# Optimization experiments

Measured on AMD Instinct MI355X. Metric: run time of the kernel, lower is better.

The kernel has to match this reference:

```python
import jax, jax.numpy as jnp
import numpy as np

N_NODES = 50000
N_EDGES = 800000
IN_DIM = 128
HIDDEN = 128
NUM_CLASSES = 2
NUM_GRAPHS = 512


def _linear_params(key, fan_in, fan_out):
    # torch nn.Linear default init: U(-1/sqrt(fan_in), 1/sqrt(fan_in))
    k1, k2 = jax.random.split(key)
    bound = 1.0 / np.sqrt(fan_in)
    W = jax.random.uniform(k1, (fan_in, fan_out), jnp.float32, -bound, bound)
    b = jax.random.uniform(k2, (fan_out,), jnp.float32, -bound, bound)
    return W, b


def setup_inputs() -> dict:
    key = jax.random.key(0)
    ks = jax.random.split(key, 8)
    x = jax.random.normal(ks[0], (N_NODES, IN_DIM), jnp.float32)
    edge_index = jax.random.randint(ks[1], (2, N_EDGES), 0, N_NODES, jnp.int64)
    batch = jnp.sort(jax.random.randint(ks[2], (N_NODES,), 0, NUM_GRAPHS, jnp.int64))
    W1a, b1a = _linear_params(ks[3], IN_DIM, HIDDEN)
    W1b, b1b = _linear_params(ks[4], HIDDEN, HIDDEN)
    W2a, b2a = _linear_params(ks[5], HIDDEN, HIDDEN)
    W2b, b2b = _linear_params(ks[6], HIDDEN, HIDDEN)
    Wfc, bfc = _linear_params(ks[7], HIDDEN, NUM_CLASSES)
    return {"x": x, "edge_index": edge_index, "batch": batch,
            "W1a": W1a, "b1a": b1a, "W1b": W1b, "b1b": b1b,
            "W2a": W2a, "b2a": b2a, "W2b": W2b, "b2b": b2b,
            "Wfc": Wfc, "bfc": bfc}


def _gin_layer(x, src, dst, Wa, ba, Wb, bb):
    # GINConv (eps=0): h_i = MLP(x_i + sum_{j->i} x_j)
    agg = jax.ops.segment_sum(x[src], dst, num_segments=N_NODES)
    h = x + agg
    h = jax.nn.relu(h @ Wa + ba)
    h = h @ Wb + bb
    return jax.nn.relu(h)  # outer F.relu in forward; dropout is identity (eval)


def reference(x, edge_index, batch, W1a, b1a, W1b, b1b, W2a, b2a, W2b, b2b, Wfc, bfc):
    src, dst = edge_index[0], edge_index[1]
    h = _gin_layer(x, src, dst, W1a, b1a, W1b, b1b)
    h = _gin_layer(h, src, dst, W2a, b2a, W2b, b2b)
    # global mean pool per graph
    sums = jax.ops.segment_sum(h, batch, num_segments=NUM_GRAPHS)
    counts = jax.ops.segment_sum(jnp.ones((N_NODES,), h.dtype), batch, num_segments=NUM_GRAPHS)
    g_emb = sums / jnp.maximum(counts, 1.0)[:, None]
    return g_emb @ Wfc + bfc  # [NUM_GRAPHS, NUM_CLASSES]
```

## Files before the change

### kernel.cpp

```cpp
#include <hip/hip_runtime.h>

typedef unsigned short ushort_t;
typedef unsigned int uint_t;

typedef __bf16 bf16x8 __attribute__((ext_vector_type(8)));
typedef float f32x4 __attribute__((ext_vector_type(4)));

#define N_NODES 50000
#define N_EDGES 800000
#define DIM 128
#define NUM_GRAPHS 512
#define LDA 136

#define ELL_CAP 64

#define NBUCK 256
#define BUCK_SZ 196
#define FIFO_CAP 4096
#define A_CHUNK 2048
#define A_BLOCKS ((N_EDGES + A_CHUNK - 1) / A_CHUNK)

#define PREP_X_BLOCKS 6250
#define PREP_W_BLOCKS 256
#define PREP_B_BLOCKS 196
#define PREP_TOTAL (A_BLOCKS + PREP_X_BLOCKS + PREP_W_BLOCKS + PREP_B_BLOCKS + 1)

__device__ __forceinline__ float bf2f(ushort_t u) {
    return __uint_as_float(((uint_t)u) << 16);
}
__device__ __forceinline__ ushort_t f2bf(float f) {
    uint_t u = __float_as_uint(f);
    u = (u + 0x7FFF + ((u >> 16) & 1)) >> 16;
    return (ushort_t)u;
}
__device__ __forceinline__ bf16x8 as_bf16x8(uint4 v) {
    return __builtin_bit_cast(bf16x8, v);
}

__global__ void zero_detect_kernel(float* gsum, int* gcnt, const void* xraw,
                                   const void* eiraw, int* flags) {
    int i = blockIdx.x * 256 + threadIdx.x;
    if (i < NUM_GRAPHS * DIM) gsum[i] = 0.f;
    if (i < NBUCK) gcnt[i] = 0;
    if (i == 0) {
        const ushort_t* u = (const ushort_t*)xraw;
        int extreme = 0;
        for (int k = 0; k < 128; ++k) {
            int e = (u[k] >> 7) & 0xFF;
            if (e >= 0xC0) extreme++;
        }
        flags[0] = (extreme > 8) ? 1 : 0;
        const int* p = (const int*)eiraw;
        int nonzero = 0;
        for (int k = 1; k < 64; k += 2) nonzero += (p[k] != 0);
        flags[1] = (nonzero == 0) ? 1 : 0;
    }
}

__global__ __launch_bounds__(256) void prep_all_kernel(
    const void* xraw, const void* braw, const void* eiraw,
    const void* W0, const void* W1, const void* W2, const void* W3,
    const void* pb1a, const void* pb1b, const void* pb2a, const void* pb2b,
    const void* pWfc, const void* pbfc, const int* __restrict__ flags,
    ushort_t* __restrict__ xout, ushort_t* __restrict__ wpout,
    int* __restrict__ batch32, float* __restrict__ params,
    int* __restrict__ gcnt, uint_t* __restrict__ fifo) {
    __shared__ int lcnt[NBUCK];
    __shared__ int lbase[NBUCK];
    int b = blockIdx.x;
    int tid = threadIdx.x;
    if (b < A_BLOCKS) {
        lcnt[tid] = 0;
        __syncthreads();
        const int* p = (const int*)eiraw;
        int i64 = flags[1];
        int base_e = b * A_CHUNK;
        int gk[8], rk[8];
        uint_t pk[8];
#pragma unroll
        for (int k = 0; k < 8; ++k) {
            int e = base_e + k * 256 + tid;
            int valid = e < N_EDGES;
            int s = 0, d = 0;
            if (valid) {
                if (i64) { s = p[2 * e]; d = p[2 * (N_EDGES + e)]; }
                else     { s = p[e];     d = p[N_EDGES + e]; }
            }
            int g = d / BUCK_SZ;
            gk[k] = valid ? g : -1;
            pk[k] = (uint_t)s | ((uint_t)(d - g * BUCK_SZ) << 16);
            rk[k] = valid ? atomicAdd(&lcnt[g], 1) : 0;
        }
        __syncthreads();
        lbase[tid] = atomicAdd(&gcnt[tid], lcnt[tid]);
        __syncthreads();
#pragma unroll
        for (int k = 0; k < 8; ++k) {
            if (gk[k] >= 0) {
                int pos = lbase[gk[k]] + rk[k];
                if (pos < FIFO_CAP)
                    fifo[(size_t)gk[k] * FIFO_CAP + pos] = pk[k];
            }
        }
    } else if (b < A_BLOCKS + PREP_X_BLOCKS) {
        if (flags[0]) {
            int i = (b - A_BLOCKS) * 256 + tid;
            if (i < N_NODES * DIM / 4) {
                float4 v = ((const float4*)xraw)[i];
                ushort4 o;
                o.x = f2bf(v.x); o.y = f2bf(v.y); o.z = f2bf(v.z); o.w = f2bf(v.w);
                ((ushort4*)xout)[i] = o;
            }
        }
    } else if (b < A_BLOCKS + PREP_X_BLOCKS + PREP_W_BLOCKS) {
        int gidx = (b - A_BLOCKS - PREP_X_BLOCKS) * 256 + tid;
        int which = gidx >> 14;
        const void* W = (which == 0) ? W0 : (which == 1) ? W1 : (which == 2) ? W2 : W3;
        int idx = gidx & 16383;
        int j = idx & 7;
        int L = (idx >> 3) & 63;
        int t = (idx >> 9) & 7;
        int s = idx >> 12;
        int k = s * 32 + (L >> 4) * 8 + j;
        int n = t * 16 + (L & 15);
        int off = k * DIM + n;
        wpout[gidx] = flags[0] ? f2bf(((const float*)W)[off]) : ((const ushort_t*)W)[off];
    } else if (b < A_BLOCKS + PREP_X_BLOCKS + PREP_W_BLOCKS + PREP_B_BLOCKS) {
        int i = (b - A_BLOCKS - PREP_X_BLOCKS - PREP_W_BLOCKS) * 256 + tid;
        if (i < N_NODES) {
            const int* p = (const int*)braw;
            batch32[i] = flags[1] ? p[2 * i] : p[i];
        }
    } else {
        for (int i = tid; i < 770; i += 256) {
            const void* srcp;
            int j;
            if (i < 128)      { srcp = pb1a; j = i; }
            else if (i < 256) { srcp = pb1b; j = i - 128; }
            else if (i < 384) { srcp = pb2a; j = i - 256; }
            else if (i < 512) { srcp = pb2b; j = i - 384; }
            else if (i < 768) { srcp = pWfc; j = i - 512; }
            else              { srcp = pbfc; j = i - 768; }
            params[i] = flags[0] ? ((const float*)srcp)[j] : bf2f(((const ushort_t*)srcp)[j]);
        }
    }
}

__global__ __launch_bounds__(256) void scatter_kernel(const uint_t* __restrict__ fifo,
                                                      const int* __restrict__ gcnt,
                                                      int* __restrict__ cnt,
                                                      int* __restrict__ ell) {
    __shared__ int lcnt[BUCK_SZ];
    int b = blockIdx.x;
    int tid = threadIdx.x;
    if (tid < BUCK_SZ) lcnt[tid] = 0;
    __syncthreads();
    int n = gcnt[b];
    if (n > FIFO_CAP) n = FIFO_CAP;
    const uint_t* f = fifo + (size_t)b * FIFO_CAP;
    int node0 = b * BUCK_SZ;
    for (int i = tid; i < n; i += 256) {
        uint_t e = f[i];
        int s = (int)(e & 0xFFFFu);
        int dl = (int)(e >> 16);
        int slot = atomicAdd(&lcnt[dl], 1);
        if (slot < ELL_CAP) ell[(size_t)(node0 + dl) * ELL_CAP + slot] = s;
    }
    __syncthreads();
    if (tid < BUCK_SZ) {
        int node = node0 + tid;
        if (node < N_NODES) cnt[node] = lcnt[tid];
    }
}

__global__ __launch_bounds__(256) void agg_kernel(const ushort_t* __restrict__ featA,
                                                  const void* __restrict__ featB,
                                                  const int* __restrict__ flags,
                                                  const int* __restrict__ deg,
                                                  const int* __restrict__ ell,
                                                  ushort_t* __restrict__ hout) {
    int n = blockIdx.x * 16 + (threadIdx.x >> 4);
    int lane = threadIdx.x & 15;
    if (n >= N_NODES) return;
    const ushort_t* feat = featA;
    if (flags && !flags[0]) feat = (const ushort_t*)featB;
    const uint4* fp = reinterpret_cast<const uint4*>(feat);
    uint4 v = fp[(size_t)n * 16 + lane];
    float a0 = bf2f((ushort_t)(v.x & 0xffff));
    float a1 = bf2f((ushort_t)(v.x >> 16));
    float a2 = bf2f((ushort_t)(v.y & 0xffff));
    float a3 = bf2f((ushort_t)(v.y >> 16));
    float a4 = bf2f((ushort_t)(v.z & 0xffff));
    float a5 = bf2f((ushort_t)(v.z >> 16));
    float a6 = bf2f((ushort_t)(v.w & 0xffff));
    float a7 = bf2f((ushort_t)(v.w >> 16));
    int e1 = deg[n];
    if (e1 > ELL_CAP) e1 = ELL_CAP;
    const int4* __restrict__ rp4 = reinterpret_cast<const int4*>(ell + (size_t)n * ELL_CAP);
    const int* __restrict__ row = ell + (size_t)n * ELL_CAP;
    int j = 0;
#define ACC8(V) \
    a0 += bf2f((ushort_t)((V).x & 0xffff)); a1 += bf2f((ushort_t)((V).x >> 16)); \
    a2 += bf2f((ushort_t)((V).y & 0xffff)); a3 += bf2f((ushort_t)((V).y >> 16)); \
    a4 += bf2f((ushort_t)((V).z & 0xffff)); a5 += bf2f((ushort_t)((V).z >> 16)); \
    a6 += bf2f((ushort_t)((V).w & 0xffff)); a7 += bf2f((ushort_t)((V).w >> 16));
    for (; j + 8 <= e1; j += 8) {
        int4 ra = rp4[j >> 2];
        int4 rb = rp4[(j >> 2) + 1];
        uint4 g0 = fp[(size_t)ra.x * 16 + lane];
        uint4 g1 = fp[(size_t)ra.y * 16 + lane];
        uint4 g2 = fp[(size_t)ra.z * 16 + lane];
        uint4 g3 = fp[(size_t)ra.w * 16 + lane];
        uint4 g4 = fp[(size_t)rb.x * 16 + lane];
        uint4 g5 = fp[(size_t)rb.y * 16 + lane];
        uint4 g6 = fp[(size_t)rb.z * 16 + lane];
        uint4 g7 = fp[(size_t)rb.w * 16 + lane];
        ACC8(g0) ACC8(g1) ACC8(g2) ACC8(g3)
        ACC8(g4) ACC8(g5) ACC8(g6) ACC8(g7)
    }
    for (; j + 4 <= e1; j += 4) {
        int4 ra = rp4[j >> 2];
        uint4 g0 = fp[(size_t)ra.x * 16 + lane];
        uint4 g1 = fp[(size_t)ra.y * 16 + lane];
        uint4 g2 = fp[(size_t)ra.z * 16 + lane];
        uint4 g3 = fp[(size_t)ra.w * 16 + lane];
        ACC8(g0) ACC8(g1) ACC8(g2) ACC8(g3)
    }
    for (; j < e1; ++j) {
        int s = row[j];
        uint4 g0 = fp[(size_t)s * 16 + lane];
        ACC8(g0)
    }
#undef ACC8
    uint4 o;
    o.x = (uint_t)f2bf(a0) | ((uint_t)f2bf(a1) << 16);
    o.y = (uint_t)f2bf(a2) | ((uint_t)f2bf(a3) << 16);
    o.z = (uint_t)f2bf(a4) | ((uint_t)f2bf(a5) << 16);
    o.w = (uint_t)f2bf(a6) | ((uint_t)f2bf(a7) << 16);
    reinterpret_cast<uint4*>(hout)[(size_t)n * 16 + lane] = o;
}

__global__ __launch_bounds__(256) void mlp_kernel(const ushort_t* __restrict__ hin,
                                                  const ushort_t* __restrict__ wpA,
                                                  const float* __restrict__ ba,
                                                  const ushort_t* __restrict__ wpB,
                                                  const float* __restrict__ bb,
                                                  ushort_t* __restrict__ hout) {
    __shared__ ushort_t As[64 * LDA];
    int tid = threadIdx.x;
    int wave = tid >> 6;
    int lane = tid & 63;
    int quad = lane >> 4;
    int cl = lane & 15;
    int row0 = blockIdx.x * 64;

    bf16x8 B1[2][4], B2[2][4];
#pragma unroll
    for (int ti = 0; ti < 2; ++ti) {
        int t = 2 * wave + ti;
#pragma unroll
        for (int s = 0; s < 4; ++s) {
            B1[ti][s] = as_bf16x8(reinterpret_cast<const uint4*>(wpA)[(s * 8 + t) * 64 + lane]);
            B2[ti][s] = as_bf16x8(reinterpret_cast<const uint4*>(wpB)[(s * 8 + t) * 64 + lane]);
        }
    }

    for (int i = tid; i < 64 * 16; i += 256) {
        int r = i >> 4, c8 = i & 15;
        uint4 v = make_uint4(0u, 0u, 0u, 0u);
        int gr = row0 + r;
        if (gr < N_NODES)
            v = reinterpret_cast<const uint4*>(hin + (size_t)gr * DIM)[c8];
        *reinterpret_cast<uint4*>(&As[r * LDA + c8 * 8]) = v;
    }
    __syncthreads();

    f32x4 acc[4][2];
#pragma unroll
    for (int m = 0; m < 4; ++m)
#pragma unroll
        for (int ti = 0; ti < 2; ++ti)
#pragma unroll
            for (int r = 0; r < 4; ++r) acc[m][ti][r] = 0.f;

#pragma unroll
    for (int s = 0; s < 4; ++s) {
#pragma unroll
        for (int m = 0; m < 4; ++m) {
            bf16x8 a = *reinterpret_cast<const bf16x8*>(&As[(m * 16 + cl) * LDA + s * 32 + quad * 8]);
#pragma unroll
            for (int ti = 0; ti < 2; ++ti)
                acc[m][ti] = __builtin_amdgcn_mfma_f32_16x16x32_bf16(a, B1[ti][s], acc[m][ti], 0, 0, 0);
        }
    }
    __syncthreads();

#pragma unroll
    for (int ti = 0; ti < 2; ++ti) {
        int col = 32 * wave + ti * 16 + cl;
        float bv = ba[col];
#pragma unroll
        for (int m = 0; m < 4; ++m)
#pragma unroll
            for (int r = 0; r < 4; ++r) {
                float v = acc[m][ti][r] + bv;
                As[(m * 16 + quad * 4 + r) * LDA + col] = f2bf(fmaxf(v, 0.f));
            }
    }
    __syncthreads();

#pragma unroll
    for (int m = 0; m < 4; ++m)
#pragma unroll
        for (int ti = 0; ti < 2; ++ti)
#pragma unroll
            for (int r = 0; r < 4; ++r) acc[m][ti][r] = 0.f;

#pragma unroll
    for (int s = 0; s < 4; ++s) {
#pragma unroll
        for (int m = 0; m < 4; ++m) {
            bf16x8 a = *reinterpret_cast<const bf16x8*>(&As[(m * 16 + cl) * LDA + s * 32 + quad * 8]);
#pragma unroll
            for (int ti = 0; ti < 2; ++ti)
                acc[m][ti] = __builtin_amdgcn_mfma_f32_16x16x32_bf16(a, B2[ti][s], acc[m][ti], 0, 0, 0);
        }
    }

#pragma unroll
    for (int ti = 0; ti < 2; ++ti) {
        int col = 32 * wave + ti * 16 + cl;
        float bv = bb[col];
#pragma unroll
        for (int m = 0; m < 4; ++m)
#pragma unroll
            for (int r = 0; r < 4; ++r) {
                int gr = row0 + m * 16 + quad * 4 + r;
                if (gr < N_NODES) {
                    float v = acc[m][ti][r] + bv;
                    hout[(size_t)gr * DIM + col] = f2bf(fmaxf(v, 0.f));
                }
            }
    }
}

__global__ __launch_bounds__(256) void mlp_pool_kernel(const ushort_t* __restrict__ hin,
                                                       const ushort_t* __restrict__ wpA,
                                                       const float* __restrict__ ba,
                                                       const ushort_t* __restrict__ wpB,
                                                       const float* __restrict__ bb,
                                                       const int* __restrict__ batch32,
                                                       float* __restrict__ gsum) {
    __shared__ ushort_t As[64 * LDA];
    int tid = threadIdx.x;
    int wave = tid >> 6;
    int lane = tid & 63;
    int quad = lane >> 4;
    int cl = lane & 15;
    int row0 = blockIdx.x * 64;

    bf16x8 B1[2][4], B2[2][4];
#pragma unroll
    for (int ti = 0; ti < 2; ++ti) {
        int t = 2 * wave + ti;
#pragma unroll
        for (int s = 0; s < 4; ++s) {
            B1[ti][s] = as_bf16x8(reinterpret_cast<const uint4*>(wpA)[(s * 8 + t) * 64 + lane]);
            B2[ti][s] = as_bf16x8(reinterpret_cast<const uint4*>(wpB)[(s * 8 + t) * 64 + lane]);
        }
    }

    for (int i = tid; i < 64 * 16; i += 256) {
        int r = i >> 4, c8 = i & 15;
        uint4 v = make_uint4(0u, 0u, 0u, 0u);
        int gr = row0 + r;
        if (gr < N_NODES)
            v = reinterpret_cast<const uint4*>(hin + (size_t)gr * DIM)[c8];
        *reinterpret_cast<uint4*>(&As[r * LDA + c8 * 8]) = v;
    }
    __syncthreads();

    f32x4 acc[4][2];
#pragma unroll
    for (int m = 0; m < 4; ++m)
#pragma unroll
        for (int ti = 0; ti < 2; ++ti)
#pragma unroll
            for (int r = 0; r < 4; ++r) acc[m][ti][r] = 0.f;

#pragma unroll
    for (int s = 0; s < 4; ++s) {
#pragma unroll
        for (int m = 0; m < 4; ++m) {
            bf16x8 a = *reinterpret_cast<const bf16x8*>(&As[(m * 16 + cl) * LDA + s * 32 + quad * 8]);
#pragma unroll
            for (int ti = 0; ti < 2; ++ti)
                acc[m][ti] = __builtin_amdgcn_mfma_f32_16x16x32_bf16(a, B1[ti][s], acc[m][ti], 0, 0, 0);
        }
    }
    __syncthreads();

#pragma unroll
    for (int ti = 0; ti < 2; ++ti) {
        int col = 32 * wave + ti * 16 + cl;
        float bv = ba[col];
#pragma unroll
        for (int m = 0; m < 4; ++m)
#pragma unroll
            for (int r = 0; r < 4; ++r) {
                float v = acc[m][ti][r] + bv;
                As[(m * 16 + quad * 4 + r) * LDA + col] = f2bf(fmaxf(v, 0.f));
            }
    }
    __syncthreads();

#pragma unroll
    for (int m = 0; m < 4; ++m)
#pragma unroll
        for (int ti = 0; ti < 2; ++ti)
#pragma unroll
            for (int r = 0; r < 4; ++r) acc[m][ti][r] = 0.f;

#pragma unroll
    for (int s = 0; s < 4; ++s) {
#pragma unroll
        for (int m = 0; m < 4; ++m) {
            bf16x8 a = *reinterpret_cast<const bf16x8*>(&As[(m * 16 + cl) * LDA + s * 32 + quad * 8]);
#pragma unroll
            for (int ti = 0; ti < 2; ++ti)
                acc[m][ti] = __builtin_amdgcn_mfma_f32_16x16x32_bf16(a, B2[ti][s], acc[m][ti], 0, 0, 0);
        }
    }
    __syncthreads();

#pragma unroll
    for (int ti = 0; ti < 2; ++ti) {
        int col = 32 * wave + ti * 16 + cl;
        float bv = bb[col];
#pragma unroll
        for (int m = 0; m < 4; ++m)
#pragma unroll
            for (int r = 0; r < 4; ++r) {
                float v = acc[m][ti][r] + bv;
                As[(m * 16 + quad * 4 + r) * LDA + col] = f2bf(fmaxf(v, 0.f));
            }
    }
    __syncthreads();

    int c = tid & 127;
    int rbase = (tid >> 7) * 32;
    float accp = 0.f;
    int curg = -1;
    for (int r = rbase; r < rbase + 32; ++r) {
        int gr = row0 + r;
        if (gr >= N_NODES) break;
        int g = batch32[gr];
        if (g != curg) {
            if (curg >= 0) atomicAdd(&gsum[curg * DIM + c], accp);
            curg = g;
            accp = 0.f;
        }
        accp += bf2f(As[r * LDA + c]);
    }
    if (curg >= 0) atomicAdd(&gsum[curg * DIM + c], accp);
}

__global__ __launch_bounds__(64) void fc_kernel(const float* __restrict__ gsum,
                                                const int* __restrict__ batch,
                                                const float* __restrict__ params,
                                                const int* __restrict__ flags,
                                                void* __restrict__ out) {
    int g = blockIdx.x;
    int l = threadIdx.x;
    int lo = 0, hi = N_NODES;
    while (lo < hi) { int mid = (lo + hi) >> 1; if (batch[mid] < g) lo = mid + 1; else hi = mid; }
    int start = lo;
    hi = N_NODES;
    while (lo < hi) { int mid = (lo + hi) >> 1; if (batch[mid] < g + 1) lo = mid + 1; else hi = mid; }
    int cnt = lo - start;
    float inv = 1.0f / (float)(cnt > 0 ? cnt : 1);
    float m0 = gsum[g * DIM + l] * inv;
    float m1 = gsum[g * DIM + 64 + l] * inv;
    float p0 = m0 * params[512 + l * 2 + 0] + m1 * params[512 + (64 + l) * 2 + 0];
    float p1 = m0 * params[512 + l * 2 + 1] + m1 * params[512 + (64 + l) * 2 + 1];
#pragma unroll
    for (int off = 32; off > 0; off >>= 1) {
        p0 += __shfl_down(p0, off, 64);
        p1 += __shfl_down(p1, off, 64);
    }
    if (l == 0) {
        float o0 = p0 + params[768];
        float o1 = p1 + params[769];
        if (flags[0]) {
            ((float*)out)[g * 2 + 0] = o0;
            ((float*)out)[g * 2 + 1] = o1;
        } else {
            ((ushort_t*)out)[g * 2 + 0] = f2bf(o0);
            ((ushort_t*)out)[g * 2 + 1] = f2bf(o1);
        }
    }
}

extern "C" void kernel_launch(void* const* d_in, const int* in_sizes, int n_in,
                              void* d_out, int out_size, void* d_ws, size_t ws_size,
                              hipStream_t stream) {
    const void* x = d_in[0];
    const void* ei = d_in[1];
    const void* batch = d_in[2];
    const void* W1a = d_in[3];
    const void* b1a = d_in[4];
    const void* W1b = d_in[5];
    const void* b1b = d_in[6];
    const void* W2a = d_in[7];
    const void* b2a = d_in[8];
    const void* W2b = d_in[9];
    const void* b2b = d_in[10];
    const void* Wfc = d_in[11];
    const void* bfc = d_in[12];

    char* base = (char*)d_ws;
    ushort_t* hX = (ushort_t*)base;   base += (size_t)N_NODES * DIM * 2;
    ushort_t* hA = (ushort_t*)base;   base += (size_t)N_NODES * DIM * 2;
    int* ell = (int*)base;            base += (size_t)N_NODES * ELL_CAP * 4;
    uint_t* fifo = (uint_t*)base;     base += (size_t)NBUCK * FIFO_CAP * 4;
    int* cnt = (int*)base;            base += (size_t)N_NODES * 4;
    int* batch32 = (int*)base;        base += (size_t)N_NODES * 4;
    int* gcnt = (int*)base;           base += NBUCK * 4;
    ushort_t* wp = (ushort_t*)base;   base += 4 * 16384 * 2;
    float* params = (float*)base;     base += 772 * 4;
    float* gsum = (float*)base;       base += (size_t)NUM_GRAPHS * DIM * 4;
    int* flags = (int*)base;          base += 16;

    ushort_t* wpA1 = wp;
    ushort_t* wpB1 = wp + 16384;
    ushort_t* wpA2 = wp + 2 * 16384;
    ushort_t* wpB2 = wp + 3 * 16384;

    zero_detect_kernel<<<256, 256, 0, stream>>>(gsum, gcnt, x, ei, flags);
    prep_all_kernel<<<PREP_TOTAL, 256, 0, stream>>>(x, batch, ei, W1a, W1b, W2a, W2b,
                                                    b1a, b1b, b2a, b2b, Wfc, bfc, flags,
                                                    hX, wp, batch32, params, gcnt, fifo);
    scatter_kernel<<<NBUCK, 256, 0, stream>>>(fifo, gcnt, cnt, ell);

    agg_kernel<<<(N_NODES + 15) / 16, 256, 0, stream>>>(hX, x, flags, cnt, ell, hA);
    mlp_kernel<<<(N_NODES + 63) / 64, 256, 0, stream>>>(hA, wpA1, params + 0, wpB1, params + 128, hA);
    agg_kernel<<<(N_NODES + 15) / 16, 256, 0, stream>>>(hA, hA, nullptr, cnt, ell, hX);
    mlp_pool_kernel<<<(N_NODES + 63) / 64, 256, 0, stream>>>(hX, wpA2, params + 256, wpB2, params + 384,
                                                             batch32, gsum);
    fc_kernel<<<NUM_GRAPHS, 64, 0, stream>>>(gsum, batch32, params, flags, d_out);
}
```

Baseline: 228.2 us.

## Store ELL neighbor lists as sorted 16-bit indices built in shared memory

The scatter kernel now assembles each bucket's neighbor lists in shared memory and insertion-sorts each row so gathers walk source nodes in ascending order. It then writes them out as 16-bit indices with coalesced 32-bit stores, which halves the adjacency footprint read by both aggregation passes. Zeroing of the pooled-sum buffer moves from the detect kernel into the scatter kernel, so the detect kernel launches with a single block. The per-row serial insertion sort adds latency to the scatter step. The ELL write now covers all 64 slots per node, including unused ones.

```diff
diff --git a/kernel.cpp b/kernel.cpp
--- a/kernel.cpp
+++ b/kernel.cpp
@@ -16,6 +16,7 @@
 
 #define NBUCK 256
 #define BUCK_SZ 196
+#define LROW 66
 #define FIFO_CAP 4096
 #define A_CHUNK 2048
 #define A_BLOCKS ((N_EDGES + A_CHUNK - 1) / A_CHUNK)
@@ -37,10 +38,9 @@
     return __builtin_bit_cast(bf16x8, v);
 }
 
-__global__ void zero_detect_kernel(float* gsum, int* gcnt, const void* xraw,
+__global__ void zero_detect_kernel(int* gcnt, const void* xraw,
                                    const void* eiraw, int* flags) {
-    int i = blockIdx.x * 256 + threadIdx.x;
-    if (i < NUM_GRAPHS * DIM) gsum[i] = 0.f;
+    int i = threadIdx.x;
     if (i < NBUCK) gcnt[i] = 0;
     if (i == 0) {
         const ushort_t* u = (const ushort_t*)xraw;
@@ -149,27 +149,52 @@
 __global__ __launch_bounds__(256) void scatter_kernel(const uint_t* __restrict__ fifo,
                                                       const int* __restrict__ gcnt,
                                                       int* __restrict__ cnt,
-                                                      int* __restrict__ ell) {
+                                                      ushort_t* __restrict__ ell,
+                                                      float* __restrict__ gsum) {
+    __shared__ ushort_t lell[BUCK_SZ][LROW];
     __shared__ int lcnt[BUCK_SZ];
     int b = blockIdx.x;
     int tid = threadIdx.x;
+    gsum[b * 256 + tid] = 0.f;
     if (tid < BUCK_SZ) lcnt[tid] = 0;
     __syncthreads();
     int n = gcnt[b];
     if (n > FIFO_CAP) n = FIFO_CAP;
     const uint_t* f = fifo + (size_t)b * FIFO_CAP;
-    int node0 = b * BUCK_SZ;
     for (int i = tid; i < n; i += 256) {
         uint_t e = f[i];
-        int s = (int)(e & 0xFFFFu);
         int dl = (int)(e >> 16);
         int slot = atomicAdd(&lcnt[dl], 1);
-        if (slot < ELL_CAP) ell[(size_t)(node0 + dl) * ELL_CAP + slot] = s;
-    }
-    __syncthreads();
+        if (slot < ELL_CAP) lell[dl][slot] = (ushort_t)(e & 0xFFFFu);
+    }
+    __syncthreads();
+    if (tid < BUCK_SZ) {
+        int deg = lcnt[tid];
+        if (deg > ELL_CAP) deg = ELL_CAP;
+        for (int i = 1; i < deg; ++i) {
+            ushort_t key = lell[tid][i];
+            int j = i - 1;
+            while (j >= 0 && lell[tid][j] > key) { lell[tid][j + 1] = lell[tid][j]; --j; }
+            lell[tid][j + 1] = key;
+        }
+    }
+    __syncthreads();
+    int node0 = b * BUCK_SZ;
+    uint_t* __restrict__ ell32 = (uint_t*)ell;
+    for (int i = tid; i < BUCK_SZ * (ELL_CAP / 2); i += 256) {
+        int dl = i >> 5;
+        int u = i & 31;
+        int node = node0 + dl;
+        if (node < N_NODES)
+            ell32[(size_t)node * (ELL_CAP / 2) + u] =
+                *reinterpret_cast<const uint_t*>(&lell[dl][2 * u]);
+    }
     if (tid < BUCK_SZ) {
         int node = node0 + tid;
-        if (node < N_NODES) cnt[node] = lcnt[tid];
+        if (node < N_NODES) {
+            int deg = lcnt[tid];
+            cnt[node] = (deg > ELL_CAP) ? ELL_CAP : deg;
+        }
     }
 }
 
@@ -177,7 +202,7 @@
                                                   const void* __restrict__ featB,
                                                   const int* __restrict__ flags,
                                                   const int* __restrict__ deg,
-                                                  const int* __restrict__ ell,
+                                                  const ushort_t* __restrict__ ell,
                                                   ushort_t* __restrict__ hout) {
     int n = blockIdx.x * 16 + (threadIdx.x >> 4);
     int lane = threadIdx.x & 15;
@@ -195,9 +220,8 @@
     float a6 = bf2f((ushort_t)(v.w & 0xffff));
     float a7 = bf2f((ushort_t)(v.w >> 16));
     int e1 = deg[n];
-    if (e1 > ELL_CAP) e1 = ELL_CAP;
-    const int4* __restrict__ rp4 = reinterpret_cast<const int4*>(ell + (size_t)n * ELL_CAP);
-    const int* __restrict__ row = ell + (size_t)n * ELL_CAP;
+    const uint4* __restrict__ rp4 = reinterpret_cast<const uint4*>(ell + (size_t)n * ELL_CAP);
+    const ushort_t* __restrict__ row = ell + (size_t)n * ELL_CAP;
     int j = 0;
 #define ACC8(V) \
     a0 += bf2f((ushort_t)((V).x & 0xffff)); a1 += bf2f((ushort_t)((V).x >> 16)); \
@@ -205,29 +229,35 @@
     a4 += bf2f((ushort_t)((V).z & 0xffff)); a5 += bf2f((ushort_t)((V).z >> 16)); \
     a6 += bf2f((ushort_t)((V).w & 0xffff)); a7 += bf2f((ushort_t)((V).w >> 16));
     for (; j + 8 <= e1; j += 8) {
-        int4 ra = rp4[j >> 2];
-        int4 rb = rp4[(j >> 2) + 1];
-        uint4 g0 = fp[(size_t)ra.x * 16 + lane];
-        uint4 g1 = fp[(size_t)ra.y * 16 + lane];
-        uint4 g2 = fp[(size_t)ra.z * 16 + lane];
-        uint4 g3 = fp[(size_t)ra.w * 16 + lane];
-        uint4 g4 = fp[(size_t)rb.x * 16 + lane];
-        uint4 g5 = fp[(size_t)rb.y * 16 + lane];
-        uint4 g6 = fp[(size_t)rb.z * 16 + lane];
-        uint4 g7 = fp[(size_t)rb.w * 16 + lane];
+        uint4 ra = rp4[j >> 3];
+        int s0 = (int)(ra.x & 0xffff), s1 = (int)(ra.x >> 16);
+        int s2 = (int)(ra.y & 0xffff), s3 = (int)(ra.y >> 16);
+        int s4 = (int)(ra.z & 0xffff), s5 = (int)(ra.z >> 16);
+        int s6 = (int)(ra.w & 0xffff), s7 = (int)(ra.w >> 16);
+        uint4 g0 = fp[(size_t)s0 * 16 + lane];
+        uint4 g1 = fp[(size_t)s1 * 16 + lane];
+        uint4 g2 = fp[(size_t)s2 * 16 + lane];
+        uint4 g3 = fp[(size_t)s3 * 16 + lane];
+        uint4 g4 = fp[(size_t)s4 * 16 + lane];
+        uint4 g5 = fp[(size_t)s5 * 16 + lane];
+        uint4 g6 = fp[(size_t)s6 * 16 + lane];
+        uint4 g7 = fp[(size_t)s7 * 16 + lane];
         ACC8(g0) ACC8(g1) ACC8(g2) ACC8(g3)
         ACC8(g4) ACC8(g5) ACC8(g6) ACC8(g7)
     }
-    for (; j + 4 <= e1; j += 4) {
-        int4 ra = rp4[j >> 2];
-        uint4 g0 = fp[(size_t)ra.x * 16 + lane];
-        uint4 g1 = fp[(size_t)ra.y * 16 + lane];
-        uint4 g2 = fp[(size_t)ra.z * 16 + lane];
-        uint4 g3 = fp[(size_t)ra.w * 16 + lane];
+    if (j + 4 <= e1) {
+        uint2 ra = *reinterpret_cast<const uint2*>(row + j);
+        int s0 = (int)(ra.x & 0xffff), s1 = (int)(ra.x >> 16);
+        int s2 = (int)(ra.y & 0xffff), s3 = (int)(ra.y >> 16);
+        uint4 g0 = fp[(size_t)s0 * 16 + lane];
+        uint4 g1 = fp[(size_t)s1 * 16 + lane];
+        uint4 g2 = fp[(size_t)s2 * 16 + lane];
+        uint4 g3 = fp[(size_t)s3 * 16 + lane];
         ACC8(g0) ACC8(g1) ACC8(g2) ACC8(g3)
+        j += 4;
     }
     for (; j < e1; ++j) {
-        int s = row[j];
+        int s = (int)row[j];
         uint4 g0 = fp[(size_t)s * 16 + lane];
         ACC8(g0)
     }
@@ -521,7 +551,7 @@
     char* base = (char*)d_ws;
     ushort_t* hX = (ushort_t*)base;   base += (size_t)N_NODES * DIM * 2;
     ushort_t* hA = (ushort_t*)base;   base += (size_t)N_NODES * DIM * 2;
-    int* ell = (int*)base;            base += (size_t)N_NODES * ELL_CAP * 4;
+    ushort_t* ell = (ushort_t*)base;  base += (size_t)N_NODES * ELL_CAP * 2;
     uint_t* fifo = (uint_t*)base;     base += (size_t)NBUCK * FIFO_CAP * 4;
     int* cnt = (int*)base;            base += (size_t)N_NODES * 4;
     int* batch32 = (int*)base;        base += (size_t)N_NODES * 4;
@@ -536,11 +566,11 @@
     ushort_t* wpA2 = wp + 2 * 16384;
     ushort_t* wpB2 = wp + 3 * 16384;
 
-    zero_detect_kernel<<<256, 256, 0, stream>>>(gsum, gcnt, x, ei, flags);
+    zero_detect_kernel<<<1, 256, 0, stream>>>(gcnt, x, ei, flags);
     prep_all_kernel<<<PREP_TOTAL, 256, 0, stream>>>(x, batch, ei, W1a, W1b, W2a, W2b,
                                                     b1a, b1b, b2a, b2b, Wfc, bfc, flags,
                                                     hX, wp, batch32, params, gcnt, fifo);
-    scatter_kernel<<<NBUCK, 256, 0, stream>>>(fifo, gcnt, cnt, ell);
+    scatter_kernel<<<NBUCK, 256, 0, stream>>>(fifo, gcnt, cnt, ell, gsum);
 
     agg_kernel<<<(N_NODES + 15) / 16, 256, 0, stream>>>(hX, x, flags, cnt, ell, hA);
     mlp_kernel<<<(N_NODES + 63) / 64, 256, 0, stream>>>(hA, wpA1, params + 0, wpB1, params + 128, hA);
```

After: 266.1 us. 16.6% more time.
